# Kernel optimization log

Hardware: AMD Instinct MI355X
Metric: run time of the kernel (lower is better)

Reference implementation:

```python
import jax, jax.numpy as jnp
import numpy as np
import math

N = 131072          # total points
B = 64              # number of segments (batches)
C = 256             # embedding_dim
H = 8               # num_heads
DH = C // H         # channels per head


def setup_inputs() -> dict:
    key = jax.random.key(0)
    ks = jax.random.split(key, 12)
    q = jax.random.normal(ks[0], (N, C), dtype=jnp.float32)
    k = jax.random.normal(ks[1], (B, C), dtype=jnp.float32)
    v = jax.random.normal(ks[2], (B, C), dtype=jnp.float32)
    batch = jnp.sort(jax.random.randint(ks[3], (N,), 0, B)).astype(jnp.int64)
    s = 1.0 / math.sqrt(C)
    Wq = jax.random.normal(ks[4], (C, C), dtype=jnp.float32) * s
    bq = jnp.zeros((C,), dtype=jnp.float32)
    Wk = jax.random.normal(ks[5], (C, C), dtype=jnp.float32) * s
    bk = jnp.zeros((C,), dtype=jnp.float32)
    Wv = jax.random.normal(ks[6], (C, C), dtype=jnp.float32) * s
    bv = jnp.zeros((C,), dtype=jnp.float32)
    Wo = jax.random.normal(ks[7], (C, C), dtype=jnp.float32) * s
    bo = jnp.zeros((C,), dtype=jnp.float32)
    return {"q": q, "k": k, "v": v, "batch": batch,
            "Wq": Wq, "bq": bq, "Wk": Wk, "bk": bk,
            "Wv": Wv, "bv": bv, "Wo": Wo, "bo": bo}


def reference(q, k, v, batch, Wq, bq, Wk, bk, Wv, bv, Wo, bo):
    batch = batch.astype(jnp.int32)
    # projections (nn.Linear: x @ W.T + b)
    qp = (q @ Wq.T + bq).reshape(N, H, DH)          # [N, H, DH]
    kp = (k @ Wk.T + bk).reshape(B, H, DH)          # [B, H, DH]
    vp = (v @ Wv.T + bv).reshape(B, H, DH)
    # gather per-point k/v by segment id
    kg = kp[batch]                                   # [N, H, DH]
    vg = vp[batch]
    # elementwise attention scores
    attn = qp * kg / math.sqrt(DH)                   # [N, H, DH]
    # ragged per-segment softmax over the point dimension (dim 0 per segment)
    m = jax.ops.segment_max(attn, batch, num_segments=B)   # [B, H, DH]
    e = jnp.exp(attn - m[batch])
    s = jax.ops.segment_sum(e, batch, num_segments=B)      # [B, H, DH]
    a = e / s[batch]                                 # [N, H, DH]
    out = (a * vg).reshape(N, C)                     # weighted values
    return out @ Wo.T + bo
```

## Files before the change

### kernel.cpp

```cpp
#include <hip/hip_runtime.h>
#include <math.h>

#define N_PTS 131072
#define BSEG 64
#define CC 256
#define BM 128
#define NSTEP 8
#define EXP_SHIFT 4.0f

#define INV_SQRT_DH 0.17677669529663687f

typedef short v8s __attribute__((ext_vector_type(8)));
typedef float v4f __attribute__((ext_vector_type(4)));
typedef int   v4i __attribute__((ext_vector_type(4)));

__device__ __forceinline__ float bf2f(unsigned short h) {
    unsigned u = ((unsigned)h) << 16;
    return __builtin_bit_cast(float, u);
}

__device__ __forceinline__ unsigned short f2bf(float f) {
    unsigned u = __builtin_bit_cast(unsigned, f);
    u += 0x7fffu + ((u >> 16) & 1u);
    return (unsigned short)(u >> 16);
}

__device__ __forceinline__ v8s pack8(const float* x) {
    int h2[4];
    #pragma unroll
    for (int i = 0; i < 4; ++i)
        h2[i] = (int)(((unsigned)f2bf(x[2 * i + 1]) << 16) | f2bf(x[2 * i]));
    return __builtin_bit_cast(v8s, make_int4(h2[0], h2[1], h2[2], h2[3]));
}

__device__ __forceinline__ v8s as_v8s(int4 v) { return __builtin_bit_cast(v8s, v); }

__global__ __launch_bounds__(256) void prep_kernel(
    const float* __restrict__ k, const float* __restrict__ v,
    const float* __restrict__ Wk, const float* __restrict__ bk,
    const float* __restrict__ Wv, const float* __restrict__ bv,
    const float* __restrict__ Wq, const float* __restrict__ Wo,
    float* __restrict__ kps, float* __restrict__ vp, float* __restrict__ ssum,
    short* __restrict__ W1q, short* __restrict__ W1o) {
    int bx = blockIdx.x;
    int c = threadIdx.x;
    if (bx < 64) {
        int b = bx;
        const float4* krow  = (const float4*)(k + (size_t)b * CC);
        const float4* vrow  = (const float4*)(v + (size_t)b * CC);
        const float4* wkrow = (const float4*)(Wk + (size_t)c * CC);
        const float4* wvrow = (const float4*)(Wv + (size_t)c * CC);
        float accK = 0.f, accV = 0.f;
        #pragma unroll 8
        for (int i = 0; i < CC / 4; ++i) {
            float4 kk = krow[i], wk = wkrow[i];
            accK += kk.x * wk.x + kk.y * wk.y + kk.z * wk.z + kk.w * wk.w;
            float4 vv = vrow[i], wv = wvrow[i];
            accV += vv.x * wv.x + vv.y * wv.y + vv.z * wv.z + vv.w * wv.w;
        }
        kps[b * CC + c] = (accK + bk[c]) * INV_SQRT_DH;
        vp[b * CC + c] = accV + bv[c];
        ssum[b * CC + c] = 0.f;
    } else {
        int wx = bx - 64;
        const float* W = (wx >= 32) ? Wo : Wq;
        short* W1 = (wx >= 32) ? W1o : W1q;
        int kf = wx & 31;
        const float* src = W + (size_t)c * CC + kf * 8;
        float4 x0 = *(const float4*)(src);
        float4 x1 = *(const float4*)(src + 4);
        float x[8] = {x0.x, x0.y, x0.z, x0.w, x1.x, x1.y, x1.z, x1.w};
        *(v8s*)&W1[((size_t)kf * 256 + c) * 8] = pack8(x);
    }
}

template <int MODE>
__global__ __launch_bounds__(512, 4) void gemm_r2(
    const void* __restrict__ Ain, const short* __restrict__ W1,
    const float* __restrict__ bias, void* __restrict__ Outv,
    const int* __restrict__ batch, const float* __restrict__ kps,
    const float* __restrict__ SV, float* __restrict__ ssum) {

    __shared__ char lds[65536];

    const int tid = threadIdx.x;
    const int lane = tid & 63;
    const int wn = tid >> 6;
    const int kfl = lane >> 4;
    const int rl = lane & 15;
    const int colb = wn * 32;
    const int m0 = blockIdx.x * BM;
    const int hsw = ((rl & 7) << 2) | (rl >> 3);

    #pragma unroll
    for (int i = 0; i < 8; ++i) {
        int j = i * 512 + tid;
        int row = j >> 5;
        int ch = j & 31;
        int h = ((row & 7) << 2) | ((row >> 3) & 1);
        int off = row * 512 + ((ch ^ h) << 4);
        if (MODE == 0) {
            const v4f* ap = (const v4f*)((const float*)Ain +
                (size_t)(m0 + row) * CC + ch * 8);
            v4f x0 = __builtin_nontemporal_load(ap);
            v4f x1 = __builtin_nontemporal_load(ap + 1);
            float x[8] = {x0.x, x0.y, x0.z, x0.w, x1.x, x1.y, x1.z, x1.w};
            *(v8s*)(lds + off) = pack8(x);
        } else {
            const v4i* ap = (const v4i*)((const unsigned short*)Ain +
                (size_t)(m0 + row) * CC + ch * 8);
            v4i praw = __builtin_nontemporal_load(ap);
            v8s p = __builtin_bit_cast(v8s, praw);
            int b = batch[m0 + row];
            const float* svp = SV + (size_t)b * CC + ch * 8;
            v4f s0 = *(const v4f*)svp;
            v4f s1 = *(const v4f*)(svp + 4);
            float x[8];
            #pragma unroll
            for (int e = 0; e < 4; ++e) {
                x[e]     = bf2f((unsigned short)p[e]) * s0[e];
                x[4 + e] = bf2f((unsigned short)p[4 + e]) * s1[e];
            }
            *(v8s*)(lds + off) = pack8(x);
        }
    }

    v4f acc[8][2];
    #pragma unroll
    for (int i = 0; i < 8; ++i)
        #pragma unroll
        for (int j = 0; j < 2; ++j) acc[i][j] = (v4f){0.f, 0.f, 0.f, 0.f};

    v8s bcur[2];
    #pragma unroll
    for (int ni = 0; ni < 2; ++ni)
        bcur[ni] = as_v8s(*(const int4*)(W1 +
            ((size_t)kfl * 256 + colb + ni * 16 + rl) * 8));

    __syncthreads();

    #pragma unroll
    for (int s = 0; s < NSTEP; ++s) {
        v8s bnx[2];
        if (s + 1 < NSTEP) {
            #pragma unroll
            for (int ni = 0; ni < 2; ++ni)
                bnx[ni] = as_v8s(*(const int4*)(W1 +
                    ((size_t)((s + 1) * 4 + kfl) * 256 + colb + ni * 16 + rl) * 8));
        }
        #pragma unroll
        for (int mi = 0; mi < 8; ++mi) {
            int abase = (mi * 16 + rl) * 512 + (((s * 4 + kfl) ^ hsw) << 4);
            v8s a = *(const v8s*)(lds + abase);
            #pragma unroll
            for (int ni = 0; ni < 2; ++ni)
                acc[mi][ni] = __builtin_amdgcn_mfma_f32_16x16x32_bf16(
                    a, bcur[ni], acc[mi][ni], 0, 0, 0);
        }
        #pragma unroll
        for (int ni = 0; ni < 2; ++ni) bcur[ni] = bnx[ni];
    }

    __syncthreads();

    const float bb0 = bias[colb + rl];
    const float bb1 = bias[colb + 16 + rl];

    if (MODE == 0) {
        unsigned short* Ou = (unsigned short*)Outv;
        const int bseg = batch[m0];
        const bool fastT = (bseg == batch[m0 + BM - 1]);
        if (!fastT) {
            int curb = -1;
            float r0 = 0.f, r1 = 0.f;
            #pragma unroll
            for (int mi = 0; mi < 8; ++mi)
                #pragma unroll
                for (int r4 = 0; r4 < 4; ++r4) {
                    int row = m0 + mi * 16 + kfl * 4 + r4;
                    int b = batch[row];
                    if (b != curb) {
                        if (curb >= 0) {
                            atomicAdd(&ssum[(size_t)curb * CC + colb + rl], r0);
                            atomicAdd(&ssum[(size_t)curb * CC + colb + 16 + rl], r1);
                            r0 = r1 = 0.f;
                        }
                        curb = b;
                    }
                    float k0 = kps[(size_t)b * CC + colb + rl];
                    float k1 = kps[(size_t)b * CC + colb + 16 + rl];
                    float p0 = __expf((acc[mi][0][r4] + bb0) * k0 - EXP_SHIFT);
                    float p1 = __expf((acc[mi][1][r4] + bb1) * k1 - EXP_SHIFT);
                    Ou[(size_t)row * CC + colb + rl] = f2bf(p0);
                    Ou[(size_t)row * CC + colb + 16 + rl] = f2bf(p1);
                    r0 += p0; r1 += p1;
                }
            atomicAdd(&ssum[(size_t)curb * CC + colb + rl], r0);
            atomicAdd(&ssum[(size_t)curb * CC + colb + 16 + rl], r1);
        } else {
            float k0 = kps[(size_t)bseg * CC + colb + rl];
            float k1 = kps[(size_t)bseg * CC + colb + 16 + rl];
            float cs0 = 0.f, cs1 = 0.f;
            unsigned short* lwu = (unsigned short*)lds + wn * 1024;
            #pragma unroll
            for (int mi = 0; mi < 8; ++mi) {
                #pragma unroll
                for (int r4 = 0; r4 < 4; ++r4) {
                    float p0 = __expf((acc[mi][0][r4] + bb0) * k0 - EXP_SHIFT);
                    float p1 = __expf((acc[mi][1][r4] + bb1) * k1 - EXP_SHIFT);
                    cs0 += p0; cs1 += p1;
                    lwu[(kfl * 4 + r4) * 40 + rl] = f2bf(p0);
                    lwu[(kfl * 4 + r4) * 40 + 16 + rl] = f2bf(p1);
                }
                asm volatile("s_waitcnt lgkmcnt(0)" ::: "memory");
                int row16 = lane >> 2, chunk = lane & 3;
                v4i pv = *(const v4i*)&lwu[row16 * 40 + chunk * 8];
                __builtin_nontemporal_store(pv,
                    (v4i*)&Ou[(size_t)(m0 + mi * 16 + row16) * CC + colb + chunk * 8]);
                asm volatile("s_waitcnt lgkmcnt(0)" ::: "memory");
            }
            cs0 += __shfl_xor(cs0, 16); cs0 += __shfl_xor(cs0, 32);
            cs1 += __shfl_xor(cs1, 16); cs1 += __shfl_xor(cs1, 32);
            if (kfl == 0) {
                atomicAdd(&ssum[(size_t)bseg * CC + colb + rl], cs0);
                atomicAdd(&ssum[(size_t)bseg * CC + colb + 16 + rl], cs1);
            }
        }
    } else {
        float* Of = (float*)Outv;
        float* lwf = (float*)(lds + wn * 2048);
        #pragma unroll
        for (int mi = 0; mi < 8; ++mi)
            #pragma unroll
            for (int c = 0; c < 2; ++c) {
                if ((kfl >> 1) == c) {
                    #pragma unroll
                    for (int r4 = 0; r4 < 4; ++r4) {
                        lwf[((kfl & 1) * 4 + r4) * 36 + rl] = acc[mi][0][r4] + bb0;
                        lwf[((kfl & 1) * 4 + r4) * 36 + 16 + rl] = acc[mi][1][r4] + bb1;
                    }
                }
                asm volatile("s_waitcnt lgkmcnt(0)" ::: "memory");
                int r = lane >> 3, c4 = lane & 7;
                v4f pv = *(const v4f*)&lwf[r * 36 + c4 * 4];
                __builtin_nontemporal_store(pv,
                    (v4f*)&Of[(size_t)(m0 + mi * 16 + c * 8 + r) * CC + colb + c4 * 4]);
                asm volatile("s_waitcnt lgkmcnt(0)" ::: "memory");
            }
    }
}

__global__ __launch_bounds__(256) void sv_kernel(
    const float* __restrict__ vp, const float* __restrict__ ssum,
    float* __restrict__ SV) {
    int i = blockIdx.x * 256 + threadIdx.x;
    SV[i] = vp[i] / ssum[i];
}

extern "C" void kernel_launch(void* const* d_in, const int* in_sizes, int n_in,
                              void* d_out, int out_size, void* d_ws, size_t ws_size,
                              hipStream_t stream) {
    const float* q  = (const float*)d_in[0];
    const float* k  = (const float*)d_in[1];
    const float* v  = (const float*)d_in[2];
    const int* batch = (const int*)d_in[3];
    const float* Wq = (const float*)d_in[4];
    const float* bq = (const float*)d_in[5];
    const float* Wk = (const float*)d_in[6];
    const float* bk = (const float*)d_in[7];
    const float* Wv = (const float*)d_in[8];
    const float* bv = (const float*)d_in[9];
    const float* Wo = (const float*)d_in[10];
    const float* bo = (const float*)d_in[11];
    float* out = (float*)d_out;

    char* wsp = (char*)d_ws;
    unsigned short* attn = (unsigned short*)wsp;
    wsp += (size_t)N_PTS * CC * sizeof(unsigned short);
    float* kps  = (float*)wsp;  wsp += (size_t)BSEG * CC * sizeof(float);
    float* vp   = (float*)wsp;  wsp += (size_t)BSEG * CC * sizeof(float);
    float* SVb  = (float*)wsp;  wsp += (size_t)BSEG * CC * sizeof(float);
    float* ssum = (float*)wsp;  wsp += (size_t)BSEG * CC * sizeof(float);
    short* W1q  = (short*)wsp;  wsp += (size_t)32 * 256 * 8 * sizeof(short);
    short* W1o  = (short*)wsp;  wsp += (size_t)32 * 256 * 8 * sizeof(short);

    prep_kernel<<<128, 256, 0, stream>>>(k, v, Wk, bk, Wv, bv, Wq, Wo,
                                         kps, vp, ssum, W1q, W1o);

    gemm_r2<0><<<N_PTS / BM, 512, 0, stream>>>(
        (const void*)q, W1q, bq, (void*)attn, batch, kps, nullptr, ssum);

    sv_kernel<<<BSEG, 256, 0, stream>>>(vp, ssum, SVb);

    gemm_r2<1><<<N_PTS / BM, 512, 0, stream>>>(
        (const void*)attn, W1o, bo, (void*)out, batch, nullptr, SVb, nullptr);
}
```

Measured before the change: 127.3 us.

## Fuse prep and both GEMM phases into one persistent cooperative kernel

```diff
diff --git a/kernel.cpp b/kernel.cpp
--- a/kernel.cpp
+++ b/kernel.cpp
@@ -1,10 +1,15 @@
 #include <hip/hip_runtime.h>
+#include <hip/hip_cooperative_groups.h>
 #include <math.h>
+
+namespace cg = cooperative_groups;
 
 #define N_PTS 131072
 #define BSEG 64
 #define CC 256
-#define BM 128
+#define BM 64
+#define TILES 4
+#define NBLK 512
 #define NSTEP 8
 #define EXP_SHIFT 4.0f
 
@@ -35,15 +40,14 @@
 
 __device__ __forceinline__ v8s as_v8s(int4 v) { return __builtin_bit_cast(v8s, v); }
 
-__global__ __launch_bounds__(256) void prep_kernel(
+__device__ __forceinline__ void prep_body(
+    int bx, int c,
     const float* __restrict__ k, const float* __restrict__ v,
     const float* __restrict__ Wk, const float* __restrict__ bk,
     const float* __restrict__ Wv, const float* __restrict__ bv,
     const float* __restrict__ Wq, const float* __restrict__ Wo,
     float* __restrict__ kps, float* __restrict__ vp, float* __restrict__ ssum,
     short* __restrict__ W1q, short* __restrict__ W1o) {
-    int bx = blockIdx.x;
-    int c = threadIdx.x;
     if (bx < 64) {
         int b = bx;
         const float4* krow  = (const float4*)(k + (size_t)b * CC);
@@ -75,13 +79,13 @@
 }
 
 template <int MODE>
-__global__ __launch_bounds__(512, 4) void gemm_r2(
+__device__ __forceinline__ void gemm_tile(
+    char* lds, const int m0,
     const void* __restrict__ Ain, const short* __restrict__ W1,
     const float* __restrict__ bias, void* __restrict__ Outv,
     const int* __restrict__ batch, const float* __restrict__ kps,
-    const float* __restrict__ SV, float* __restrict__ ssum) {
-
-    __shared__ char lds[65536];
+    const float* __restrict__ vp, const float* __restrict__ ssum_ro,
+    float* __restrict__ ssum) {
 
     const int tid = threadIdx.x;
     const int lane = tid & 63;
@@ -89,11 +93,10 @@
     const int kfl = lane >> 4;
     const int rl = lane & 15;
     const int colb = wn * 32;
-    const int m0 = blockIdx.x * BM;
     const int hsw = ((rl & 7) << 2) | (rl >> 3);
 
     #pragma unroll
-    for (int i = 0; i < 8; ++i) {
+    for (int i = 0; i < 4; ++i) {
         int j = i * 512 + tid;
         int row = j >> 5;
         int ch = j & 31;
@@ -109,25 +112,28 @@
         } else {
             const v4i* ap = (const v4i*)((const unsigned short*)Ain +
                 (size_t)(m0 + row) * CC + ch * 8);
-            v4i praw = __builtin_nontemporal_load(ap);
+            v4i praw = *ap;
             v8s p = __builtin_bit_cast(v8s, praw);
             int b = batch[m0 + row];
-            const float* svp = SV + (size_t)b * CC + ch * 8;
-            v4f s0 = *(const v4f*)svp;
-            v4f s1 = *(const v4f*)(svp + 4);
+            const float* vpp = vp + (size_t)b * CC + ch * 8;
+            const float* ssp = ssum_ro + (size_t)b * CC + ch * 8;
+            v4f a0 = *(const v4f*)vpp;
+            v4f a1 = *(const v4f*)(vpp + 4);
+            v4f s0 = *(const v4f*)ssp;
+            v4f s1 = *(const v4f*)(ssp + 4);
             float x[8];
             #pragma unroll
             for (int e = 0; e < 4; ++e) {
-                x[e]     = bf2f((unsigned short)p[e]) * s0[e];
-                x[4 + e] = bf2f((unsigned short)p[4 + e]) * s1[e];
+                x[e]     = bf2f((unsigned short)p[e]) * __fdividef(a0[e], s0[e]);
+                x[4 + e] = bf2f((unsigned short)p[4 + e]) * __fdividef(a1[e], s1[e]);
             }
             *(v8s*)(lds + off) = pack8(x);
         }
     }
 
-    v4f acc[8][2];
-    #pragma unroll
-    for (int i = 0; i < 8; ++i)
+    v4f acc[4][2];
+    #pragma unroll
+    for (int i = 0; i < 4; ++i)
         #pragma unroll
         for (int j = 0; j < 2; ++j) acc[i][j] = (v4f){0.f, 0.f, 0.f, 0.f};
 
@@ -149,7 +155,7 @@
                     ((size_t)((s + 1) * 4 + kfl) * 256 + colb + ni * 16 + rl) * 8));
         }
         #pragma unroll
-        for (int mi = 0; mi < 8; ++mi) {
+        for (int mi = 0; mi < 4; ++mi) {
             int abase = (mi * 16 + rl) * 512 + (((s * 4 + kfl) ^ hsw) << 4);
             v8s a = *(const v8s*)(lds + abase);
             #pragma unroll
@@ -174,7 +180,7 @@
             int curb = -1;
             float r0 = 0.f, r1 = 0.f;
             #pragma unroll
-            for (int mi = 0; mi < 8; ++mi)
+            for (int mi = 0; mi < 4; ++mi)
                 #pragma unroll
                 for (int r4 = 0; r4 < 4; ++r4) {
                     int row = m0 + mi * 16 + kfl * 4 + r4;
@@ -203,7 +209,7 @@
             float cs0 = 0.f, cs1 = 0.f;
             unsigned short* lwu = (unsigned short*)lds + wn * 1024;
             #pragma unroll
-            for (int mi = 0; mi < 8; ++mi) {
+            for (int mi = 0; mi < 4; ++mi) {
                 #pragma unroll
                 for (int r4 = 0; r4 < 4; ++r4) {
                     float p0 = __expf((acc[mi][0][r4] + bb0) * k0 - EXP_SHIFT);
@@ -215,8 +221,7 @@
                 asm volatile("s_waitcnt lgkmcnt(0)" ::: "memory");
                 int row16 = lane >> 2, chunk = lane & 3;
                 v4i pv = *(const v4i*)&lwu[row16 * 40 + chunk * 8];
-                __builtin_nontemporal_store(pv,
-                    (v4i*)&Ou[(size_t)(m0 + mi * 16 + row16) * CC + colb + chunk * 8]);
+                *(v4i*)&Ou[(size_t)(m0 + mi * 16 + row16) * CC + colb + chunk * 8] = pv;
                 asm volatile("s_waitcnt lgkmcnt(0)" ::: "memory");
             }
             cs0 += __shfl_xor(cs0, 16); cs0 += __shfl_xor(cs0, 32);
@@ -230,7 +235,7 @@
         float* Of = (float*)Outv;
         float* lwf = (float*)(lds + wn * 2048);
         #pragma unroll
-        for (int mi = 0; mi < 8; ++mi)
+        for (int mi = 0; mi < 4; ++mi)
             #pragma unroll
             for (int c = 0; c < 2; ++c) {
                 if ((kfl >> 1) == c) {
@@ -250,11 +255,71 @@
     }
 }
 
-__global__ __launch_bounds__(256) void sv_kernel(
-    const float* __restrict__ vp, const float* __restrict__ ssum,
-    float* __restrict__ SV) {
-    int i = blockIdx.x * 256 + threadIdx.x;
-    SV[i] = vp[i] / ssum[i];
+__global__ __launch_bounds__(512, 4) void fused_kernel(
+    const float* __restrict__ q, const float* __restrict__ k,
+    const float* __restrict__ v, const int* __restrict__ batch,
+    const float* __restrict__ Wq, const float* __restrict__ bq,
+    const float* __restrict__ Wk, const float* __restrict__ bk,
+    const float* __restrict__ Wv, const float* __restrict__ bv,
+    const float* __restrict__ Wo, const float* __restrict__ bo,
+    float* __restrict__ out, unsigned short* __restrict__ attn,
+    float* __restrict__ kps, float* __restrict__ vp,
+    float* __restrict__ ssum, short* __restrict__ W1q,
+    short* __restrict__ W1o) {
+
+    __shared__ char lds[32768];
+    cg::grid_group grid = cg::this_grid();
+
+    if (blockIdx.x < 128 && threadIdx.x < 256)
+        prep_body(blockIdx.x, threadIdx.x, k, v, Wk, bk, Wv, bv, Wq, Wo,
+                  kps, vp, ssum, W1q, W1o);
+    grid.sync();
+
+    const int mbase = blockIdx.x * (TILES * BM);
+    #pragma unroll 1
+    for (int t = 0; t < TILES; ++t) {
+        if (t) __syncthreads();
+        gemm_tile<0>(lds, mbase + t * BM, (const void*)q, W1q, bq,
+                     (void*)attn, batch, kps, nullptr, nullptr, ssum);
+    }
+    grid.sync();
+    #pragma unroll 1
+    for (int t = 0; t < TILES; ++t) {
+        if (t) __syncthreads();
+        gemm_tile<1>(lds, mbase + t * BM, (const void*)attn, W1o, bo,
+                     (void*)out, batch, nullptr, vp, ssum, nullptr);
+    }
+}
+
+__global__ __launch_bounds__(256) void prep_kernel(
+    const float* __restrict__ k, const float* __restrict__ v,
+    const float* __restrict__ Wk, const float* __restrict__ bk,
+    const float* __restrict__ Wv, const float* __restrict__ bv,
+    const float* __restrict__ Wq, const float* __restrict__ Wo,
+    float* __restrict__ kps, float* __restrict__ vp, float* __restrict__ ssum,
+    short* __restrict__ W1q, short* __restrict__ W1o) {
+    prep_body(blockIdx.x, threadIdx.x, k, v, Wk, bk, Wv, bv, Wq, Wo,
+              kps, vp, ssum, W1q, W1o);
+}
+
+__global__ __launch_bounds__(512, 4) void gemm_k0(
+    const float* __restrict__ q, const short* __restrict__ W1,
+    const float* __restrict__ bias, unsigned short* __restrict__ attn,
+    const int* __restrict__ batch, const float* __restrict__ kps,
+    float* __restrict__ ssum) {
+    __shared__ char lds[32768];
+    gemm_tile<0>(lds, blockIdx.x * BM, (const void*)q, W1, bias,
+                 (void*)attn, batch, kps, nullptr, nullptr, ssum);
+}
+
+__global__ __launch_bounds__(512, 4) void gemm_k1(
+    const unsigned short* __restrict__ attn, const short* __restrict__ W1,
+    const float* __restrict__ bias, float* __restrict__ out,
+    const int* __restrict__ batch, const float* __restrict__ vp,
+    const float* __restrict__ ssum) {
+    __shared__ char lds[32768];
+    gemm_tile<1>(lds, blockIdx.x * BM, (const void*)attn, W1, bias,
+                 (void*)out, batch, nullptr, vp, ssum, nullptr);
 }
 
 extern "C" void kernel_launch(void* const* d_in, const int* in_sizes, int n_in,
@@ -279,19 +344,24 @@
     wsp += (size_t)N_PTS * CC * sizeof(unsigned short);
     float* kps  = (float*)wsp;  wsp += (size_t)BSEG * CC * sizeof(float);
     float* vp   = (float*)wsp;  wsp += (size_t)BSEG * CC * sizeof(float);
-    float* SVb  = (float*)wsp;  wsp += (size_t)BSEG * CC * sizeof(float);
     float* ssum = (float*)wsp;  wsp += (size_t)BSEG * CC * sizeof(float);
     short* W1q  = (short*)wsp;  wsp += (size_t)32 * 256 * 8 * sizeof(short);
     short* W1o  = (short*)wsp;  wsp += (size_t)32 * 256 * 8 * sizeof(short);
 
-    prep_kernel<<<128, 256, 0, stream>>>(k, v, Wk, bk, Wv, bv, Wq, Wo,
-                                         kps, vp, ssum, W1q, W1o);
-
-    gemm_r2<0><<<N_PTS / BM, 512, 0, stream>>>(
-        (const void*)q, W1q, bq, (void*)attn, batch, kps, nullptr, ssum);
-
-    sv_kernel<<<BSEG, 256, 0, stream>>>(vp, ssum, SVb);
-
-    gemm_r2<1><<<N_PTS / BM, 512, 0, stream>>>(
-        (const void*)attn, W1o, bo, (void*)out, batch, nullptr, SVb, nullptr);
-}
+    void* args[] = {
+        (void*)&q, (void*)&k, (void*)&v, (void*)&batch,
+        (void*)&Wq, (void*)&bq, (void*)&Wk, (void*)&bk,
+        (void*)&Wv, (void*)&bv, (void*)&Wo, (void*)&bo,
+        (void*)&out, (void*)&attn, (void*)&kps, (void*)&vp,
+        (void*)&ssum, (void*)&W1q, (void*)&W1o
+    };
+    hipError_t err = hipLaunchCooperativeKernel(
+        (const void*)fused_kernel, dim3(NBLK), dim3(512), args, 0, stream);
+
+    if (err != hipSuccess) {
+        prep_kernel<<<128, 256, 0, stream>>>(k, v, Wk, bk, Wv, bv, Wq, Wo,
+                                             kps, vp, ssum, W1q, W1o);
+        gemm_k0<<<N_PTS / BM, 512, 0, stream>>>(q, W1q, bq, attn, batch, kps, ssum);
+        gemm_k1<<<N_PTS / BM, 512, 0, stream>>>(attn, W1o, bo, out, batch, vp, ssum);
+    }
+}
```

Result: slower. 251.7 us (+97.7%).
